# Performance work log

Measured on AMD Instinct MI355X. Metric: run time of the kernel, lower is better.

The kernel has to match this reference:

```python
import jax, jax.numpy as jnp
import numpy as np

# Module hyperparameters (init_kwargs)
N_CLASSES = 21
RADIUS = 5
SIZE = (256, 256)
SIGMA_DIST = 4.0
SIGMA_FEAT = 1.0
B, C = 8, 32


def _offsets(radius):
    """Integer (dy, dx) offsets with Euclidean distance < radius (includes (0,0))."""
    offs = []
    r = int(radius)
    for dy in range(-r + 1, r):
        for dx in range(-r + 1, r):
            if dy * dy + dx * dx < radius * radius:
                offs.append((dy, dx))
    return offs


OFFSETS = _offsets(RADIUS)  # 69 offsets for radius=5


def setup_inputs() -> dict:
    key = jax.random.key(0)
    k1, k2 = jax.random.split(key)
    H, W = SIZE
    classification = jax.random.uniform(k1, (B, N_CLASSES, H, W), dtype=jnp.float32)
    features = jax.random.normal(k2, (B, C, H, W), dtype=jnp.float32)
    return {"classification": classification, "features": features}


def reference(classification, features):
    # classification: [B, K, H, W] soft assignments S
    # features:       [B, C, H, W]
    Bb, K, H, W = classification.shape
    inv_sd2 = 1.0 / (SIGMA_DIST * SIGMA_DIST)
    inv_sf2 = 1.0 / (SIGMA_FEAT * SIGMA_FEAT)

    hs = jnp.arange(H)
    ws = jnp.arange(W)

    WS = jnp.zeros_like(classification)           # (W @ S), [B, K, H, W]
    degree = jnp.zeros((Bb, H, W), classification.dtype)

    # Loop over the small fixed set of neighbor offsets (69 for radius=5).
    for dy, dx in OFFSETS:
        f_nb = jnp.roll(features, (-dy, -dx), axis=(2, 3))
        s_nb = jnp.roll(classification, (-dy, -dx), axis=(2, 3))
        # mask out wrap-around: neighbor (h+dy, w+dx) must be in-bounds
        valid_h = (hs + dy >= 0) & (hs + dy < H)
        valid_w = (ws + dx >= 0) & (ws + dx < W)
        mask = (valid_h[:, None] & valid_w[None, :]).astype(classification.dtype)
        # Gaussian affinity: distance kernel * feature kernel
        feat_d2 = ((features - f_nb) ** 2).sum(axis=1)        # [B, H, W]
        w = jnp.exp(-(dy * dy + dx * dx) * inv_sd2 - feat_d2 * inv_sf2) * mask
        WS = WS + w[:, None] * s_nb
        degree = degree + w

    # numerator   = S^T W S : [B, K, K]
    # denominator = d^T S   : [B, K]
    num = jnp.einsum('bkhw,bjhw->bkj', classification, WS)
    den = jnp.einsum('bhw,bkhw->bk', degree, classification)
    return (num / den[:, None, :]).sum()
```

## Files before the change

kernel.cpp:

```cpp
#include <hip/hip_runtime.h>

#define HH 256
#define WW 256
#define HWPX 65536
#define BB 8
#define KK 21
#define CC 32

typedef _Float16 half2v __attribute__((ext_vector_type(2)));
union F4H { float4 f4; half2v h[4]; };

__global__ __launch_bounds__(256) void prep(const float* __restrict__ cls,
                                            const float* __restrict__ feat,
                                            float4* __restrict__ fpk,
                                            float2* __restrict__ TN) {
    const int tid = blockIdx.x * 256 + threadIdx.x;
    const int p2 = tid * 2;
    const int b = p2 >> 16;
    const int p = p2 & (HWPX - 1);

    const float* cbase = cls + (size_t)b * KK * HWPX + p;
    float sx = 0.f, sy = 0.f;
#pragma unroll
    for (int k = 0; k < KK; ++k) {
        float2 c = *(const float2*)(cbase + (size_t)k * HWPX);
        sx += c.x; sy += c.y;
    }

    const float* src = feat + (size_t)b * CC * HWPX + p;
    float nq0 = 0.f, nq1 = 0.f;
#pragma unroll 1
    for (int j = 0; j < 4; ++j) {
        float2 ch[8];
#pragma unroll
        for (int c = 0; c < 8; ++c)
            ch[c] = *(const float2*)(src + (size_t)(j * 8 + c) * HWPX);
        F4H u0, u1;
#pragma unroll
        for (int k = 0; k < 4; ++k) {
            u0.h[k] = __builtin_bit_cast(half2v, __builtin_amdgcn_cvt_pkrtz(ch[2 * k].x, ch[2 * k + 1].x));
            nq0 = __builtin_amdgcn_fdot2(u0.h[k], u0.h[k], nq0, false);
            u1.h[k] = __builtin_bit_cast(half2v, __builtin_amdgcn_cvt_pkrtz(ch[2 * k].y, ch[2 * k + 1].y));
            nq1 = __builtin_amdgcn_fdot2(u1.h[k], u1.h[k], nq1, false);
        }
        fpk[(size_t)j * (BB * HWPX) + p2]     = u0.f4;
        fpk[(size_t)j * (BB * HWPX) + p2 + 1] = u1.f4;
    }
    TN[p2]     = make_float2(sx, nq0);
    TN[p2 + 1] = make_float2(sy, nq1);
}

__global__ __launch_bounds__(256) void affinity5(const float4* __restrict__ fpk,
                                                 const float2* __restrict__ TN,
                                                 const float* __restrict__ cls,
                                                 float* __restrict__ numer,
                                                 float* __restrict__ denom) {
    __shared__ float smV[1024], smD[1024];
    __shared__ float pN[4][22], pD[4][22];

    const int L  = blockIdx.x;
    const int b  = L & 7;
    const int t  = L >> 3;
    const int by = t & 15;
    const int bx = t >> 4;
    const int lane = threadIdx.x & 63;
    const int wid  = threadIdx.x >> 6;
    const int gx  = bx * 64 + lane;
    const int gy0 = by * 16 + wid * 4;

    const size_t bofs = (size_t)b * HWPX;
    const float4* fb0 = fpk + bofs;
    const float4* fb1 = fpk + (size_t)1 * BB * HWPX + bofs;
    const float4* fb2 = fpk + (size_t)2 * BB * HWPX + bofs;
    const float4* fb3 = fpk + (size_t)3 * BB * HWPX + bofs;
    const float2* tnb = TN + bofs;

    F4H fp[4][4];
    float np_[4];
#pragma unroll
    for (int py = 0; py < 4; ++py) {
        const int pp = ((gy0 + py) << 8) | gx;
        fp[py][0].f4 = fb0[pp];
        fp[py][1].f4 = fb1[pp];
        fp[py][2].f4 = fb2[pp];
        fp[py][3].f4 = fb3[pp];
        np_[py] = tnb[pp].y;
    }

    float degacc[4] = {0.f, 0.f, 0.f, 0.f};
    float vacc[4]   = {0.f, 0.f, 0.f, 0.f};

#pragma unroll 1
    for (int dyi = 0; dyi < 12; ++dyi) {
        const int ny = gy0 + dyi - 4;
        if ((unsigned)ny >= HH) continue;
        const int rowq = ny << 8;

        int dy2[4];
        float base[4];
#pragma unroll
        for (int py = 0; py < 4; ++py) {
            const int d = dyi - 4 - py;
            dy2[py] = d * d;
            base[py] = fmaf(-0.03125f, (float)dy2[py], -0.5f * np_[py]);
        }
        const int mind = min(min(dy2[0], dy2[1]), min(dy2[2], dy2[3]));

#pragma unroll 3
        for (int dxi = 0; dxi < 9; ++dxi) {
            const int dx = dxi - 4;
            const int dx2 = dx * dx;
            if (mind + dx2 >= 25) continue;

            const int gx2 = gx + dx;
            const bool vx = (unsigned)gx2 < WW;
            const int q = rowq | min(max(gx2, 0), WW - 1);

            F4H nb0, nb1, nb2, nb3;
            nb0.f4 = fb0[q];
            nb1.f4 = fb1[q];
            nb2.f4 = fb2[q];
            nb3.f4 = fb3[q];
            const float2 tq = tnb[q];
            const float cdx = (float)dx2 * -0.03125f;

#pragma unroll
            for (int py = 0; py < 4; ++py) {
                if (dy2[py] + dx2 < 25) {
                    float acc = fmaf(-0.5f, tq.y, base[py] + cdx);
#pragma unroll
                    for (int k = 0; k < 4; ++k) {
                        acc = __builtin_amdgcn_fdot2(fp[py][0].h[k], nb0.h[k], acc, false);
                        acc = __builtin_amdgcn_fdot2(fp[py][1].h[k], nb1.h[k], acc, false);
                        acc = __builtin_amdgcn_fdot2(fp[py][2].h[k], nb2.h[k], acc, false);
                        acc = __builtin_amdgcn_fdot2(fp[py][3].h[k], nb3.h[k], acc, false);
                    }
                    float w = __builtin_exp2f(acc * 2.8853900817779268f);
                    w = vx ? w : 0.f;
                    degacc[py] += w;
                    vacc[py] = fmaf(w, tq.x, vacc[py]);
                }
            }
        }
    }

#pragma unroll
    for (int py = 0; py < 4; ++py) {
        const int li = ((wid * 4 + py) << 6) | lane;
        smV[li] = vacc[py];
        smD[li] = degacc[py];
    }
    __syncthreads();

    const int li0 = threadIdx.x * 4;
    const int lr  = li0 >> 6;
    const int lc  = li0 & 63;
    const int gp  = ((by * 16 + lr) << 8) | (bx * 64 + lc);
    const float4 v4 = *(const float4*)&smV[li0];
    const float4 d4 = *(const float4*)&smD[li0];
    const float* clsb = cls + (size_t)b * KK * HWPX + gp;

    float accN[KK], accD[KK];
#pragma unroll 7
    for (int j = 0; j < KK; ++j) {
        float4 s4 = *(const float4*)(clsb + (size_t)j * HWPX);
        float n = s4.x * v4.x;   n = fmaf(s4.y, v4.y, n);
        n = fmaf(s4.z, v4.z, n); n = fmaf(s4.w, v4.w, n);
        float d = s4.x * d4.x;   d = fmaf(s4.y, d4.y, d);
        d = fmaf(s4.z, d4.z, d); d = fmaf(s4.w, d4.w, d);
        accN[j] = n; accD[j] = d;
    }

#pragma unroll
    for (int j = 0; j < KK; ++j) {
        float n = accN[j], d = accD[j];
#pragma unroll
        for (int off = 32; off > 0; off >>= 1) {
            n += __shfl_down(n, off);
            d += __shfl_down(d, off);
        }
        if (lane == 0) { pN[wid][j] = n; pD[wid][j] = d; }
    }
    __syncthreads();
    if (threadIdx.x < 2 * KK) {
        int half = threadIdx.x / KK;
        int j = threadIdx.x - half * KK;
        float acc = half ? (pD[0][j] + pD[1][j] + pD[2][j] + pD[3][j])
                         : (pN[0][j] + pN[1][j] + pN[2][j] + pN[3][j]);
        float* dst = half ? denom : numer;
        atomicAdd(&dst[b * KK + j], acc);
    }
}

__global__ __launch_bounds__(256) void finalize(const float* __restrict__ numer,
                                                const float* __restrict__ denom,
                                                float* __restrict__ out) {
    __shared__ float sm[4];
    int i = threadIdx.x;
    float r = 0.f;
    if (i < BB * KK) r = numer[i] / denom[i];
#pragma unroll
    for (int off = 32; off > 0; off >>= 1) r += __shfl_down(r, off);
    if ((i & 63) == 0) sm[i >> 6] = r;
    __syncthreads();
    if (i == 0) out[0] = sm[0] + sm[1] + sm[2] + sm[3];
}

extern "C" void kernel_launch(void* const* d_in, const int* in_sizes, int n_in,
                              void* d_out, int out_size, void* d_ws, size_t ws_size,
                              hipStream_t stream) {
    const float* cls  = (const float*)d_in[0];
    const float* feat = (const float*)d_in[1];
    float* out = (float*)d_out;

    const size_t BHW = (size_t)BB * HWPX;
    float4* fpk   = (float4*)d_ws;
    float2* TN    = (float2*)((char*)d_ws + BHW * 64);
    float*  numer = (float*)((char*)TN + BHW * 8);
    float*  denom = numer + BB * KK;

    (void)hipMemsetAsync(numer, 0, 2 * BB * KK * sizeof(float), stream);
    prep<<<dim3(BHW / 512), dim3(256), 0, stream>>>(cls, feat, fpk, TN);
    affinity5<<<dim3(512), dim3(256), 0, stream>>>(fpk, TN, cls, numer, denom);
    finalize<<<dim3(1), dim3(256), 0, stream>>>(numer, denom, out);
}
```

Baseline: 206.5 us.

## Split affinity rows across two blocks and fold memset/finalize into kernels

The affinity kernel now launches twice as many blocks, and each block handles half of the vertical neighbor offsets, so more of the GPU is occupied. The accumulator memset moves into the prep kernel, and the finalize kernel is replaced by a last-block-done pattern using an atomic counter. Together these remove one memset and one kernel launch. The costs are that the per-block epilogue over the classification tensor and the atomics now run twice, and prep processes one pixel per thread instead of two.

Measured after the change: 213.1 us. +3.2%, slower.

```diff
diff --git a/kernel.cpp b/kernel.cpp
--- a/kernel.cpp
+++ b/kernel.cpp
@@ -6,6 +6,8 @@
 #define BB 8
 #define KK 21
 #define CC 32
+#define NOUT (BB * KK)
+#define AFF_BLOCKS 1024
 
 typedef _Float16 half2v __attribute__((ext_vector_type(2)));
 union F4H { float4 f4; half2v h[4]; };
@@ -13,60 +15,63 @@
 __global__ __launch_bounds__(256) void prep(const float* __restrict__ cls,
                                             const float* __restrict__ feat,
                                             float4* __restrict__ fpk,
-                                            float2* __restrict__ TN) {
+                                            float2* __restrict__ TN,
+                                            float* __restrict__ accum ) {
+    if (blockIdx.x == 0) {
+        for (int i = threadIdx.x; i < NOUT * 2 + 1; i += 256)
+            ((unsigned*)accum)[i] = 0u;
+    }
+
     const int tid = blockIdx.x * 256 + threadIdx.x;
-    const int p2 = tid * 2;
-    const int b = p2 >> 16;
-    const int p = p2 & (HWPX - 1);
+    const int b = tid >> 16;
+    const int p = tid & (HWPX - 1);
 
     const float* cbase = cls + (size_t)b * KK * HWPX + p;
-    float sx = 0.f, sy = 0.f;
-#pragma unroll
-    for (int k = 0; k < KK; ++k) {
-        float2 c = *(const float2*)(cbase + (size_t)k * HWPX);
-        sx += c.x; sy += c.y;
-    }
+    float s = 0.f;
+#pragma unroll
+    for (int k = 0; k < KK; ++k) s += cbase[(size_t)k * HWPX];
 
     const float* src = feat + (size_t)b * CC * HWPX + p;
-    float nq0 = 0.f, nq1 = 0.f;
+    float nq = 0.f;
 #pragma unroll 1
     for (int j = 0; j < 4; ++j) {
-        float2 ch[8];
-#pragma unroll
-        for (int c = 0; c < 8; ++c)
-            ch[c] = *(const float2*)(src + (size_t)(j * 8 + c) * HWPX);
-        F4H u0, u1;
+        float ch[8];
+#pragma unroll
+        for (int c = 0; c < 8; ++c) ch[c] = src[(size_t)(j * 8 + c) * HWPX];
+        F4H u;
 #pragma unroll
         for (int k = 0; k < 4; ++k) {
-            u0.h[k] = __builtin_bit_cast(half2v, __builtin_amdgcn_cvt_pkrtz(ch[2 * k].x, ch[2 * k + 1].x));
-            nq0 = __builtin_amdgcn_fdot2(u0.h[k], u0.h[k], nq0, false);
-            u1.h[k] = __builtin_bit_cast(half2v, __builtin_amdgcn_cvt_pkrtz(ch[2 * k].y, ch[2 * k + 1].y));
-            nq1 = __builtin_amdgcn_fdot2(u1.h[k], u1.h[k], nq1, false);
-        }
-        fpk[(size_t)j * (BB * HWPX) + p2]     = u0.f4;
-        fpk[(size_t)j * (BB * HWPX) + p2 + 1] = u1.f4;
-    }
-    TN[p2]     = make_float2(sx, nq0);
-    TN[p2 + 1] = make_float2(sy, nq1);
+            u.h[k] = __builtin_bit_cast(half2v, __builtin_amdgcn_cvt_pkrtz(ch[2 * k], ch[2 * k + 1]));
+            nq = __builtin_amdgcn_fdot2(u.h[k], u.h[k], nq, false);
+        }
+        fpk[(size_t)j * (BB * HWPX) + tid] = u.f4;
+    }
+    TN[tid] = make_float2(s, nq);
 }
 
-__global__ __launch_bounds__(256) void affinity5(const float4* __restrict__ fpk,
+__global__ __launch_bounds__(256) void affinity6(const float4* __restrict__ fpk,
                                                  const float2* __restrict__ TN,
                                                  const float* __restrict__ cls,
                                                  float* __restrict__ numer,
-                                                 float* __restrict__ denom) {
+                                                 float* __restrict__ denom,
+                                                 unsigned* __restrict__ counter,
+                                                 float* __restrict__ out) {
     __shared__ float smV[1024], smD[1024];
     __shared__ float pN[4][22], pD[4][22];
-
-    const int L  = blockIdx.x;
-    const int b  = L & 7;
-    const int t  = L >> 3;
-    const int by = t & 15;
-    const int bx = t >> 4;
+    __shared__ float sm[4];
+    __shared__ unsigned sdone;
+
+    const int L    = blockIdx.x;
+    const int b    = L & 7;
+    const int rest = L >> 3;
+    const int half = rest & 1;
+    const int t    = rest >> 1;
+    const int by   = t & 15;
+    const int bx   = t >> 4;
     const int lane = threadIdx.x & 63;
     const int wid  = threadIdx.x >> 6;
-    const int gx  = bx * 64 + lane;
-    const int gy0 = by * 16 + wid * 4;
+    const int gx   = bx * 64 + lane;
+    const int gy0  = by * 16 + wid * 4;
 
     const size_t bofs = (size_t)b * HWPX;
     const float4* fb0 = fpk + bofs;
@@ -90,8 +95,11 @@
     float degacc[4] = {0.f, 0.f, 0.f, 0.f};
     float vacc[4]   = {0.f, 0.f, 0.f, 0.f};
 
+    const int dy_lo = half * 6;
+    const int dy_hi = dy_lo + 6;
+
 #pragma unroll 1
-    for (int dyi = 0; dyi < 12; ++dyi) {
+    for (int dyi = dy_lo; dyi < dy_hi; ++dyi) {
         const int ny = gy0 + dyi - 4;
         if ((unsigned)ny >= HH) continue;
         const int rowq = ny << 8;
@@ -183,27 +191,34 @@
     }
     __syncthreads();
     if (threadIdx.x < 2 * KK) {
-        int half = threadIdx.x / KK;
-        int j = threadIdx.x - half * KK;
-        float acc = half ? (pD[0][j] + pD[1][j] + pD[2][j] + pD[3][j])
-                         : (pN[0][j] + pN[1][j] + pN[2][j] + pN[3][j]);
-        float* dst = half ? denom : numer;
+        int h2 = threadIdx.x / KK;
+        int j = threadIdx.x - h2 * KK;
+        float acc = h2 ? (pD[0][j] + pD[1][j] + pD[2][j] + pD[3][j])
+                       : (pN[0][j] + pN[1][j] + pN[2][j] + pN[3][j]);
+        float* dst = h2 ? denom : numer;
         atomicAdd(&dst[b * KK + j], acc);
     }
-}
-
-__global__ __launch_bounds__(256) void finalize(const float* __restrict__ numer,
-                                                const float* __restrict__ denom,
-                                                float* __restrict__ out) {
-    __shared__ float sm[4];
-    int i = threadIdx.x;
-    float r = 0.f;
-    if (i < BB * KK) r = numer[i] / denom[i];
-#pragma unroll
-    for (int off = 32; off > 0; off >>= 1) r += __shfl_down(r, off);
-    if ((i & 63) == 0) sm[i >> 6] = r;
+
+    if (threadIdx.x == 0) {
+        __threadfence();
+        unsigned old = atomicAdd(counter, 1u);
+        sdone = (old == (unsigned)(AFF_BLOCKS - 1)) ? 1u : 0u;
+    }
     __syncthreads();
-    if (i == 0) out[0] = sm[0] + sm[1] + sm[2] + sm[3];
+    if (sdone) {
+        const int i = threadIdx.x;
+        float r = 0.f;
+        if (i < NOUT) {
+            float n = atomicAdd(&numer[i], 0.f);
+            float d = atomicAdd(&denom[i], 0.f);
+            r = n / d;
+        }
+#pragma unroll
+        for (int off = 32; off > 0; off >>= 1) r += __shfl_down(r, off);
+        if ((i & 63) == 0) sm[i >> 6] = r;
+        __syncthreads();
+        if (i == 0) out[0] = sm[0] + sm[1] + sm[2] + sm[3];
+    }
 }
 
 extern "C" void kernel_launch(void* const* d_in, const int* in_sizes, int n_in,
@@ -214,13 +229,12 @@
     float* out = (float*)d_out;
 
     const size_t BHW = (size_t)BB * HWPX;
-    float4* fpk   = (float4*)d_ws;
-    float2* TN    = (float2*)((char*)d_ws + BHW * 64);
-    float*  numer = (float*)((char*)TN + BHW * 8);
-    float*  denom = numer + BB * KK;
-
-    (void)hipMemsetAsync(numer, 0, 2 * BB * KK * sizeof(float), stream);
-    prep<<<dim3(BHW / 512), dim3(256), 0, stream>>>(cls, feat, fpk, TN);
-    affinity5<<<dim3(512), dim3(256), 0, stream>>>(fpk, TN, cls, numer, denom);
-    finalize<<<dim3(1), dim3(256), 0, stream>>>(numer, denom, out);
+    float4*   fpk     = (float4*)d_ws;
+    float2*   TN      = (float2*)((char*)d_ws + BHW * 64);
+    float*    numer   = (float*)((char*)TN + BHW * 8);
+    float*    denom   = numer + NOUT;
+    unsigned* counter = (unsigned*)(denom + NOUT);
+
+    prep<<<dim3(BHW / 256), dim3(256), 0, stream>>>(cls, feat, fpk, TN, numer);
+    affinity6<<<dim3(AFF_BLOCKS), dim3(256), 0, stream>>>(fpk, TN, cls, numer, denom, counter, out);
 }
```
